# Optimization experiments

Measured on AMD Instinct MI355X. Metric: run time of the kernel, lower is better.

## Reference

```python
import jax, jax.numpy as jnp
import numpy as np

B, E, F, Q = 16, 2048, 8192, 20
D, WD = 256, 300
NUM_ENTITY, NUM_WORD, NUM_RELATION = 100000, 50000, 600
NUM_LAYER = 3
PAGERANK_LAMBDA = 0.8
FACT_SCALE = 3.0
VERY_NEG = -100000000000.0
VERY_SMALL = 1e-10


def setup_inputs() -> dict:
    key = jax.random.key(0)
    ks = jax.random.split(key, 40)
    s = 0.05
    L = NUM_LAYER
    inp = {
        'local_entity': jax.random.randint(ks[0], (B, E), 0, NUM_ENTITY),
        'q2e_adj_mat': jax.random.uniform(ks[1], (B, E, 1), jnp.float32),
        'kb_fact_rel': jax.random.randint(ks[2], (B, F), 0, NUM_RELATION),
        'query_text': jax.random.randint(ks[3], (B, Q), 0, NUM_WORD),
        'answer_dist': jax.random.uniform(ks[4], (B, E), jnp.float32),
        'e2f_ent': jax.random.randint(ks[5], (B, F), 0, E),
        'f2e_ent': jax.random.randint(ks[6], (B, F), 0, E),
        'word_emb': jax.random.normal(ks[7], (NUM_WORD + 1, WD)) * s,
        'entity_emb': jax.random.normal(ks[8], (NUM_ENTITY + 1, WD)) * s,
        'relation_emb': jax.random.normal(ks[9], (NUM_RELATION + 1, 2 * WD)) * s,
        'entity_lin_w': jax.random.normal(ks[10], (D, WD)) * s,
        'entity_lin_b': jnp.zeros((D,)),
        'relation_lin_w': jax.random.normal(ks[11], (D, 2 * WD)) * s,
        'relation_lin_b': jnp.zeros((D,)),
        'lstm_w_ih': jax.random.normal(ks[12], (4 * D, WD)) * s,
        'lstm_w_hh': jax.random.normal(ks[13], (4 * D, D)) * s,
        'lstm_b_ih': jnp.zeros((4 * D,)),
        'lstm_b_hh': jnp.zeros((4 * D,)),
        'q2e_w': jax.random.normal(ks[14], (L, D, D)) * s,
        'q2e_b': jnp.zeros((L, D)),
        'e2q_w': jax.random.normal(ks[15], (L, D, 3 * D)) * s,
        'e2q_b': jnp.zeros((L, D)),
        'e2e_w': jax.random.normal(ks[16], (L, D, 3 * D)) * s,
        'e2e_b': jnp.zeros((L, D)),
        'kb_head_w': jax.random.normal(ks[17], (L, D, D)) * s,
        'kb_head_b': jnp.zeros((L, D)),
        'kb_tail_w': jax.random.normal(ks[18], (L, D, D)) * s,
        'kb_tail_b': jnp.zeros((L, D)),
        'kb_self_w': jax.random.normal(ks[19], (L, D, D)) * s,
        'kb_self_b': jnp.zeros((L, D)),
        'score_w': jax.random.normal(ks[20], (1, D)) * s,
        'score_b': jnp.zeros((1,)),
    }
    return inp


def _lstm(x, w_ih, w_hh, b_ih, b_hh):
    # torch LSTM, single layer, unidirectional, zero init state; gates (i,f,g,o)
    gx = jnp.einsum('btd,gd->btg', x, w_ih) + b_ih + b_hh  # [B,T,4H]
    H = w_hh.shape[1]
    init = (jnp.zeros((x.shape[0], H), x.dtype), jnp.zeros((x.shape[0], H), x.dtype))
    def step(carry, g):
        h, c = carry
        z = g + h @ w_hh.T
        i, f, gg, o = jnp.split(z, 4, axis=-1)
        c = jax.nn.sigmoid(f) * c + jax.nn.sigmoid(i) * jnp.tanh(gg)
        h = jax.nn.sigmoid(o) * jnp.tanh(c)
        return (h, c), h
    (h, _), hs = jax.lax.scan(step, init, jnp.swapaxes(gx, 0, 1))
    return jnp.swapaxes(hs, 0, 1), h  # [B,T,H], [B,H]


def _forward(local_entity, q2e_adj_mat, kb_fact_rel, query_text, e2f_ent, f2e_ent,
             word_emb, entity_emb, relation_emb,
             entity_lin_w, entity_lin_b, relation_lin_w, relation_lin_b,
             lstm_w_ih, lstm_w_hh, lstm_b_ih, lstm_b_hh,
             q2e_w, q2e_b, e2q_w, e2q_b, e2e_w, e2e_b,
             kb_head_w, kb_head_b, kb_tail_w, kb_tail_b, kb_self_w, kb_self_b,
             score_w, score_b):
    bidx = jnp.arange(B)[:, None]
    ent_mask = (local_entity != NUM_ENTITY).astype(jnp.float32)  # [B,E]
    q_mask = (query_text != NUM_WORD).astype(jnp.float32)        # [B,Q]

    # query LSTM encoding (dropout = identity in eval)
    qh, qlast = _lstm(word_emb[query_text], lstm_w_ih, lstm_w_hh, lstm_b_ih, lstm_b_hh)
    query_node = qlast[:, None, :]                               # [B,1,D]

    # fact embeddings
    lf = relation_emb[kb_fact_rel] @ relation_lin_w.T + relation_lin_b  # [B,F,D]
    div = jnp.sqrt(jnp.float32(D))

    # fact <-> query attention
    sim = jnp.einsum('bqd,bfd->bqf', qh, lf) / div
    sim = jax.nn.softmax(sim + (1.0 - q_mask)[:, :, None] * VERY_NEG, axis=1)
    att = jnp.einsum('bqf,bqd->bfd', sim, qh)
    Wf = jnp.sum(att * lf, axis=2) / div                          # [B,F]
    W_tilde = jnp.exp(Wf - jnp.max(Wf, axis=1, keepdims=True))    # [B,F]

    # e2f softmax normalizer: scatter-add fact weights onto head entities
    e2f_softmax = jnp.zeros((B, E), W_tilde.dtype).at[bidx, e2f_ent].add(W_tilde)
    e2f_softmax = jnp.maximum(e2f_softmax, VERY_SMALL)

    # entity embeddings (word_dim != entity_dim -> linear projection)
    le = entity_emb[local_entity] @ entity_lin_w.T + entity_lin_b  # [B,E,D]
    pagerank = q2e_adj_mat[..., 0]                                 # [B,E]

    for i in range(NUM_LAYER):
        q2e = jnp.broadcast_to(query_node @ q2e_w[i].T + q2e_b[i], (B, E, D))
        # fact update: self + gathered head-entity messages
        fact_self = lf @ kb_self_w[i].T + kb_self_b[i]
        head = le @ kb_head_w[i].T + kb_head_b[i]
        e2f_emb = jax.nn.relu(fact_self + jnp.take_along_axis(head, e2f_ent[:, :, None], axis=1))
        norm = W_tilde * jnp.take_along_axis(pagerank / e2f_softmax, e2f_ent, axis=1)  # [B,F]
        e2f_emb = e2f_emb * norm[:, :, None]
        # entity update: self + scattered tail messages
        tail = e2f_emb @ kb_tail_w[i].T + kb_tail_b[i]
        ent_self = le @ kb_self_w[i].T + kb_self_b[i]
        f2e_emb = jax.nn.relu(ent_self + jnp.zeros((B, E, D), le.dtype).at[bidx, f2e_ent].add(tail))
        pagerank = (PAGERANK_LAMBDA * jnp.zeros((B, E), norm.dtype).at[bidx, f2e_ent].add(norm)
                    + (1.0 - PAGERANK_LAMBDA) * pagerank)
        nxt = jnp.concatenate([le, q2e, FACT_SCALE * f2e_emb], axis=2)  # [B,E,3D]
        query_node = jnp.einsum('be,bed->bd', pagerank, nxt @ e2q_w[i].T + e2q_b[i])[:, None, :]
        le = jax.nn.relu(nxt @ e2e_w[i].T + e2e_b[i])

    score = (le @ score_w.T + score_b)[..., 0]                     # [B,E]
    return score


def reference(local_entity, q2e_adj_mat, kb_fact_rel, query_text, answer_dist,
              e2f_ent, f2e_ent, word_emb, entity_emb, relation_emb,
              entity_lin_w, entity_lin_b, relation_lin_w, relation_lin_b,
              lstm_w_ih, lstm_w_hh, lstm_b_ih, lstm_b_hh,
              q2e_w, q2e_b, e2q_w, e2q_b, e2e_w, e2e_b,
              kb_head_w, kb_head_b, kb_tail_w, kb_tail_b, kb_self_w, kb_self_b,
              score_w, score_b):
    return _forward(local_entity, q2e_adj_mat, kb_fact_rel, query_text, e2f_ent, f2e_ent,
                    word_emb, entity_emb, relation_emb,
                    entity_lin_w, entity_lin_b, relation_lin_w, relation_lin_b,
                    lstm_w_ih, lstm_w_hh, lstm_b_ih, lstm_b_hh,
                    q2e_w, q2e_b, e2q_w, e2q_b, e2e_w, e2e_b,
                    kb_head_w, kb_head_b, kb_tail_w, kb_tail_b, kb_self_w, kb_self_b,
                    score_w, score_b)
```

## Files before the change

### kernel.cpp

```cpp
#include <hip/hip_runtime.h>
#include <hip/hip_bf16.h>

typedef __hip_bfloat16 bf16;
typedef __attribute__((ext_vector_type(8))) short bf16x8;
typedef __attribute__((ext_vector_type(4))) float f32x4;

#define BB 16
#define EE 2048
#define FF 8192
#define QQ 20
#define DD 256
#define WDIM 300
#define NWORD 50000
#define VERY_NEG_F (-1.0e11f)

static __device__ __forceinline__ float b2f(bf16 x){ return __bfloat162float(x); }
static __device__ __forceinline__ bf16 f2b(float x){ return __float2bfloat16(x); }
static __device__ __forceinline__ float sigm(float x){ return 1.f/(1.f+expf(-x)); }
static __device__ __forceinline__ void ld4bf(const bf16* p, float v[4]){
  short4 s = *(const short4*)p;
  v[0]=b2f(*(const bf16*)&s.x); v[1]=b2f(*(const bf16*)&s.y);
  v[2]=b2f(*(const bf16*)&s.z); v[3]=b2f(*(const bf16*)&s.w);
}
static __device__ __forceinline__ void st4bf(bf16* p, float a,float b,float c,float d){
  unsigned short u[4]; bf16 t;
  t=f2b(a);u[0]=*(unsigned short*)&t; t=f2b(b);u[1]=*(unsigned short*)&t;
  t=f2b(c);u[2]=*(unsigned short*)&t; t=f2b(d);u[3]=*(unsigned short*)&t;
  *(short4*)p=*(short4*)u;
}

#define O_GX       0UL
#define O_QH       1310720UL
#define O_QNODE    1638400UL
#define O_RELLIN   1654784UL
#define O_WR       2270208UL
#define O_WMAX     2308864UL
#define O_WT       2309120UL
#define O_E2FS     2833408UL
#define O_PR       2964480UL
#define O_PRAGG    3095552UL
#define O_Q2EV     3226624UL
#define O_Q2EVB    3243008UL
#define O_RELSELF  3251200UL
#define O_NORM     3866624UL
#define O_WNXT     4390912UL
#define O_PRSUM    4440064UL
#define O_CNT      4440320UL
#define O_CUR      4571392UL
#define O_BSTART   4702464UL
#define O_BIDX     4834048UL
#define O_ELWPAD   5358336UL
#define O_FLAG     5522176UL
#define O_CVT      5522432UL
#define O_AGG      10915584UL
#define O_ENTSELF  27692800UL
#define O_LEA      44470016UL
#define O_LEB      61247232UL
#define O_HEAD     78024448UL
#define O_F2EEMB   94801664UL

#define C_ELB   0
#define C_RLW   256
#define C_RLB   153856
#define C_WIH   154112
#define C_WHH   461312
#define C_BIH   723456
#define C_BHH   724480
#define C_Q2EW  725504
#define C_Q2EB  922112
#define C_E2QW  922880
#define C_E2QB  1512704
#define C_E2EW  1513472
#define C_E2EB  2103296
#define C_KHW   2104064
#define C_KHB   2300672
#define C_KTW   2301440
#define C_KTB   2498048
#define C_KSW   2498816
#define C_KSB   2695424
#define C_SCW   2696192
#define C_SCB   2696448

__global__ __launch_bounds__(256) void k_sniff(const unsigned short* ee, int* flag){
  __shared__ int red[256];
  int c=0;
  for(int i=threadIdx.x;i<4096;i+=256){
    int ex=(ee[2*i]>>7)&0xFF;
    c += (ex>=192);
  }
  red[threadIdx.x]=c; __syncthreads();
  for(int o=128;o;o>>=1){ if(threadIdx.x<o) red[threadIdx.x]+=red[threadIdx.x+o]; __syncthreads(); }
  if(!threadIdx.x) flag[0] = (red[0]>64) ? 1 : 0;
}

struct CvtJobs{ const void* src[20]; bf16* dst[20]; int n[20]; int sc[20]; };
__global__ __launch_bounds__(256) void k_cvt(CvtJobs J, const int* dfl){
  const int isf=*dfl;
  int j=blockIdx.y;
  int n=J.n[j];
  int i4=(blockIdx.x*256+threadIdx.x)*4;
  if(i4>=n) return;
  float m = (J.sc[j] && ((i4%768)>=512)) ? 3.f : 1.f;
  bf16* d=J.dst[j]+i4;
  if(isf){
    const float* s=(const float*)J.src[j]+i4;
    if(i4+4<=n){ float4 t=*(const float4*)s; st4bf(d,t.x*m,t.y*m,t.z*m,t.w*m); }
    else for(int r=0;i4+r<n;r++) d[r]=f2b(s[r]*m);
  } else {
    const bf16* s=(const bf16*)J.src[j]+i4;
    if(i4+4<=n){ float v[4]; ld4bf(s,v); st4bf(d,v[0]*m,v[1]*m,v[2]*m,v[3]*m); }
    else for(int r=0;i4+r<n;r++) d[r]=f2b(b2f(s[r])*m);
  }
}

__global__ __launch_bounds__(256) void k_cvtwhh(const void* src, bf16* wf, const int* dfl){
  const int isf=*dfl;
  int fid=blockIdx.x*256+threadIdx.x;
  int lane=fid&63, kt=(fid>>6)&7, gt=fid>>9;
  int l16=lane&15, q=lane>>4;
  long so=(long)(gt*16+l16)*256 + kt*32 + q*8;
  float v[8];
  if(isf){ const float* s=(const float*)src+so;
    #pragma unroll
    for(int j=0;j<8;j++) v[j]=s[j];
  } else { const bf16* s=(const bf16*)src+so; ld4bf(s,v); ld4bf(s+4,v+4); }
  bf16* d=wf+(long)fid*8;
  st4bf(d,v[0],v[1],v[2],v[3]); st4bf(d+4,v[4],v[5],v[6],v[7]);
}

__global__ __launch_bounds__(256) void k_cvtelw(const void* src, bf16* dst, const int* dfl){
  const int isf=*dfl;
  int r=blockIdx.x;
  for(int c=threadIdx.x;c<320;c+=256){
    float v=0.f;
    if(c<300) v = isf ? ((const float*)src)[r*300+c] : b2f(((const bf16*)src)[r*300+c]);
    dst[(long)r*320+c]=f2b(v);
  }
}

__global__ __launch_bounds__(128) void k_ga0(const int* idx, const void* emb, bf16* A0, const int* dfl){
  const int isf=*dfl;
  int row=blockIdx.x; int ent=idx[row]; int t=threadIdx.x;
  bf16* dst=A0+(long)row*320;
  if(t<75){
    float v[4];
    if(isf){ float4 x=*(const float4*)((const float*)emb+(long)ent*WDIM+t*4);
             v[0]=x.x;v[1]=x.y;v[2]=x.z;v[3]=x.w; }
    else ld4bf((const bf16*)emb+(long)ent*WDIM+t*4, v);
    st4bf(dst+t*4, v[0],v[1],v[2],v[3]);
  } else if(t<80){
    st4bf(dst+t*4, 0.f,0.f,0.f,0.f);
  }
}

__global__ __launch_bounds__(256) void k_cnt(const int* f2e, int* cnt){
  int i=blockIdx.x*256+threadIdx.x;
  atomicAdd(&cnt[((i>>13)<<11)+f2e[i]], 1);
}
__global__ __launch_bounds__(1024) void k_scan(const int* cnt, int* bstart){
  __shared__ int ps[1024];
  int t=threadIdx.x;
  int loc[32]; int s=0;
  #pragma unroll
  for(int j=0;j<32;j++){ loc[j]=s; s+=cnt[t*32+j]; }
  ps[t]=s; __syncthreads();
  for(int off=1;off<1024;off<<=1){
    int v=(t>=off)?ps[t-off]:0;
    __syncthreads(); ps[t]+=v; __syncthreads();
  }
  int base=(t? ps[t-1]:0);
  #pragma unroll
  for(int j=0;j<32;j++) bstart[t*32+j]=base+loc[j];
  if(t==1023) bstart[32768]=ps[1023];
}
__global__ __launch_bounds__(256) void k_fill(const int* f2e, const int* bstart, int* cur, int* bidx){
  int i=blockIdx.x*256+threadIdx.x;
  int key=((i>>13)<<11)+f2e[i];
  int pos=bstart[key]+atomicAdd(&cur[key],1);
  bidx[pos]=i;
}

__global__ __launch_bounds__(256) void k_gx(const int* qtext, const void* wemb,
    const bf16* wih, const bf16* bih, const bf16* bhh, float* gx, const int* dfl){
  const int isf=*dfl;
  int bt=blockIdx.x;
  __shared__ float xr[WDIM];
  int w=qtext[bt];
  for(int k4=threadIdx.x*4;k4<WDIM;k4+=1024){
    if(isf){ float4 t=*(const float4*)((const float*)wemb+(long)w*WDIM+k4);
             xr[k4]=t.x;xr[k4+1]=t.y;xr[k4+2]=t.z;xr[k4+3]=t.w; }
    else   { float v[4]; ld4bf((const bf16*)wemb+(long)w*WDIM+k4,v);
             xr[k4]=v[0];xr[k4+1]=v[1];xr[k4+2]=v[2];xr[k4+3]=v[3]; }
  }
  __syncthreads();
  #pragma unroll
  for(int s=0;s<4;s++){
    int g=threadIdx.x+256*s;
    float acc=b2f(bih[g])+b2f(bhh[g]);
    const bf16* wr=wih+(long)g*WDIM;
    for(int k4=0;k4<WDIM;k4+=4){
      float v[4]; ld4bf(wr+k4,v);
      acc+=v[0]*xr[k4]+v[1]*xr[k4+1]+v[2]*xr[k4+2]+v[3]*xr[k4+3];
    }
    gx[bt*1024+g]=acc;
  }
}

#define NLB 16
__global__ __launch_bounds__(256) void k_lstm3(const float* gx, const bf16* wf,
    float* qh, float* qnode, bf16* hbuf, int* lcnt){
  __shared__ bf16  hlds[16*264];
  __shared__ float zs[4*16*16];
  __shared__ bf16  hsl[256];
  const int k=blockIdx.x;
  const int tid=threadIdx.x;
  const int wv=tid>>6, lane=tid&63, q=lane>>4, l16=lane&15;
  const int b=tid>>4, u=tid&15, gu=k*16+u;
  bf16x8 wreg[8];
  #pragma unroll
  for(int kt=0;kt<8;kt++)
    wreg[kt]=*(const bf16x8*)(wf + (((long)((wv*16+k)*8+kt))*64 + lane)*8);
  float c=0.f;
  float gxr[4];
  #pragma unroll
  for(int g=0;g<4;g++) gxr[g]=gx[(b*QQ+0)*1024 + g*256 + gu];
  for(int t=0;t<QQ;t++){
    f32x4 acc=(f32x4){0.f,0.f,0.f,0.f};
    if(t){
      if(tid==0){
        while(__hip_atomic_load(lcnt+(t-1), __ATOMIC_ACQUIRE, __HIP_MEMORY_SCOPE_AGENT) < NLB)
          __builtin_amdgcn_s_sleep(1);
      }
      __syncthreads();
      const bf16* hb = hbuf + (t&1)*4096;
      #pragma unroll
      for(int ii=0;ii<4;ii++){
        int i=tid+ii*256;
        int r=i>>6, cc=i&63;
        unsigned long long v=__hip_atomic_load((const unsigned long long*)(hb + r*256 + cc*4),
                       __ATOMIC_RELAXED, __HIP_MEMORY_SCOPE_AGENT);
        *(unsigned long long*)&hlds[r*264 + cc*4] = v;
      }
      __syncthreads();
      #pragma unroll
      for(int kt=0;kt<8;kt++){
        bf16x8 af=*(const bf16x8*)&hlds[l16*264 + kt*32 + q*8];
        acc=__builtin_amdgcn_mfma_f32_16x16x32_bf16(af,wreg[kt],acc,0,0,0);
      }
    }
    #pragma unroll
    for(int r=0;r<4;r++) zs[wv*256 + (q*4+r)*16 + l16]=acc[r];
    __syncthreads();
    float zi=zs[0*256+tid]+gxr[0];
    float zf=zs[1*256+tid]+gxr[1];
    float zg=zs[2*256+tid]+gxr[2];
    float zo=zs[3*256+tid]+gxr[3];
    {
      int tn=(t<QQ-1)?t+1:t;
      #pragma unroll
      for(int g=0;g<4;g++) gxr[g]=gx[(b*QQ+tn)*1024 + g*256 + gu];
    }
    c=sigm(zf)*c+sigm(zi)*tanhf(zg);
    float hv=sigm(zo)*tanhf(c);
    hsl[tid]=f2b(hv);
    qh[(long)(b*QQ+t)*256+gu]=hv;
    if(t==QQ-1) qnode[(b<<8)+gu]=hv;
    __syncthreads();
    if(t<QQ-1){
      if(tid<64){
        bf16* hw=hbuf + ((t+1)&1)*4096;
        int bb=tid>>2, p=tid&3;
        unsigned long long v=*(unsigned long long*)&hsl[bb*16+p*4];
        __hip_atomic_store((unsigned long long*)(hw + bb*256 + k*16 + p*4), v,
                           __ATOMIC_RELAXED, __HIP_MEMORY_SCOPE_AGENT);
      }
      __syncthreads();
      if(tid==0){
        __threadfence();
        __hip_atomic_fetch_add(lcnt+t, 1, __ATOMIC_RELEASE, __HIP_MEMORY_SCOPE_AGENT);
      }
    }
  }
}

__global__ __launch_bounds__(256) void k_rel_lin(const void* remb, const bf16* rlw,
    const bf16* rlb, float* rel_lin, const int* dfl){
  const int isf=*dfl;
  int r=blockIdx.x;
  __shared__ float rr[2*WDIM];
  for(int k4=threadIdx.x*4;k4<2*WDIM;k4+=1024){
    if(isf){ float4 t=*(const float4*)((const float*)remb+(long)r*2*WDIM+k4);
             rr[k4]=t.x;rr[k4+1]=t.y;rr[k4+2]=t.z;rr[k4+3]=t.w; }
    else   { float v[4]; ld4bf((const bf16*)remb+(long)r*2*WDIM+k4,v);
             rr[k4]=v[0];rr[k4+1]=v[1];rr[k4+2]=v[2];rr[k4+3]=v[3]; }
  }
  __syncthreads();
  int d=threadIdx.x;
  float acc=b2f(rlb[d]);
  const bf16* wr=rlw+(long)d*2*WDIM;
  for(int k4=0;k4<2*WDIM;k4+=4){
    float v[4]; ld4bf(wr+k4,v);
    acc+=v[0]*rr[k4]+v[1]*rr[k4+1]+v[2]*rr[k4+2]+v[3]*rr[k4+3];
  }
  rel_lin[r*DD+d]=acc;
}

__global__ __launch_bounds__(256) void k_simwr(const float* qh, const float* rel_lin,
    const int* qtext, float* Wr){
  int b = blockIdx.x, rc = blockIdx.y;
  __shared__ float qhb[QQ*DD];
  __shared__ float qm[QQ];
  for(int i=threadIdx.x;i<QQ*DD;i+=256) qhb[i]=qh[b*QQ*DD+i];
  if(threadIdx.x<QQ) qm[threadIdx.x] = (qtext[b*QQ+threadIdx.x]!=NWORD)?0.f:VERY_NEG_F;
  __syncthreads();
  int r = rc*256+threadIdx.x;
  if(r>=601) return;
  float s[QQ];
  #pragma unroll
  for(int q=0;q<QQ;q++) s[q]=0.f;
  for(int k=0;k<DD;k++){
    float rl = rel_lin[r*DD+k];
    #pragma unroll
    for(int q=0;q<QQ;q++) s[q] += qhb[q*DD+k]*rl;
  }
  float m=-1e30f;
  #pragma unroll
  for(int q=0;q<QQ;q++){ s[q]*=0.0625f; m=fmaxf(m, s[q]+qm[q]); }
  float sum=0.f, w=0.f;
  #pragma unroll
  for(int q=0;q<QQ;q++){ float p=expf(s[q]+qm[q]-m); sum+=p; w+=p*s[q]; }
  Wr[b*601+r] = w/sum;
}

__global__ __launch_bounds__(256) void k_wmax(const float* Wr, const int* rel, float* wmax){
  int b=blockIdx.x; __shared__ float red[256];
  float m=-1e30f;
  for(int f=threadIdx.x;f<FF;f+=256) m=fmaxf(m, Wr[b*601+rel[b*FF+f]]);
  red[threadIdx.x]=m; __syncthreads();
  for(int o=128;o;o>>=1){ if(threadIdx.x<o) red[threadIdx.x]=fmaxf(red[threadIdx.x],red[threadIdx.x+o]); __syncthreads(); }
  if(!threadIdx.x) wmax[b]=red[0];
}
__global__ __launch_bounds__(256) void k_wt(const float* Wr, const int* rel,
    const float* wmax, const int* e2f, float* wt, float* e2fs){
  int i = blockIdx.x*256+threadIdx.x;
  int b = i>>13;
  float v = expf(Wr[b*601+rel[i]] - wmax[b]);
  wt[i]=v;
  atomicAdd(e2fs + (b<<11) + e2f[i], v);
}
__global__ __launch_bounds__(256) void k_prinit(const void* adj, float* pr, const int* dfl){
  const int isf=*dfl;
  int i4=(blockIdx.x*256+threadIdx.x)*4;
  if(isf){ *(float4*)(pr+i4)=*(const float4*)((const float*)adj+i4); }
  else { float v[4]; ld4bf((const bf16*)adj+i4,v);
         float4 t; t.x=v[0];t.y=v[1];t.z=v[2];t.w=v[3]; *(float4*)(pr+i4)=t; }
}

struct MG {
  const bf16* A; const bf16* W; const bf16* bias;
  bf16* out; int K;
  const bf16* Aq2; const bf16* Af2;
  const int* cnt; const bf16* addb;
};
template<int CONCAT,int EPI>
__global__ __launch_bounds__(256) void k_mgemm(MG p){
  const int m0 = blockIdx.x*64;
  const int wave = threadIdx.x>>6, lane = threadIdx.x&63;
  const int q = lane>>4, l16 = lane&15;
  const int n0 = wave*64;
  const int bidx_ = m0>>11;
  f32x4 acc[4][4];
  #pragma unroll
  for(int i=0;i<4;i++)
    #pragma unroll
    for(int j=0;j<4;j++) acc[i][j]=(f32x4){0.f,0.f,0.f,0.f};
  const int K=p.K;
  for(int k0=0;k0<K;k0+=32){
    int kk=k0+q*8;
    bf16x8 af[4], bw[4];
    #pragma unroll
    for(int mi=0;mi<4;mi++){
      int row=m0+mi*16+l16;
      const bf16* ap;
      if(CONCAT){
        if(kk<256)      ap=p.A  +(long)row*256+kk;
        else if(kk<512) ap=p.Aq2+(bidx_<<8)+(kk-256);
        else            ap=p.Af2+(long)row*256+(kk-512);
      } else ap=p.A+(long)row*K+kk;
      af[mi]=*(const bf16x8*)ap;
    }
    #pragma unroll
    for(int ni=0;ni<4;ni++)
      bw[ni]=*(const bf16x8*)(p.W+(long)(n0+ni*16+l16)*K+kk);
    #pragma unroll
    for(int mi=0;mi<4;mi++)
      #pragma unroll
      for(int ni=0;ni<4;ni++)
        acc[mi][ni]=__builtin_amdgcn_mfma_f32_16x16x32_bf16(af[mi],bw[ni],acc[mi][ni],0,0,0);
  }
  #pragma unroll
  for(int ni=0;ni<4;ni++){
    int col=n0+ni*16+l16;
    float bv=b2f(p.bias[col]);
    #pragma unroll
    for(int mi=0;mi<4;mi++){
      #pragma unroll
      for(int r=0;r<4;r++){
        int row=m0+mi*16+q*4+r;
        float v=acc[mi][ni][r];
        if(EPI==0) v+=bv;
        else if(EPI==1) v=fmaxf(v+bv,0.f);
        else {
          v += (float)p.cnt[row]*bv + b2f(p.addb[(long)row*256+col]);
          v=fmaxf(v,0.f);
        }
        p.out[(long)row*256+col]=f2b(v);
      }
    }
  }
}

__global__ __launch_bounds__(256) void k_small(const float* rel_lin, const bf16* selfw,
    const bf16* selfb, const float* qnode, const bf16* q2ew, const bf16* q2eb,
    float* relself, float* q2ev, bf16* q2evb){
  __shared__ float xr[DD];
  int d=threadIdx.x;
  if(blockIdx.x<601){
    int r=blockIdx.x;
    xr[d]=rel_lin[r*DD+d]; __syncthreads();
    float acc=b2f(selfb[d]);
    const bf16* wr=selfw+(long)d*DD;
    for(int k4=0;k4<DD;k4+=4){
      float v[4]; ld4bf(wr+k4,v);
      acc+=v[0]*xr[k4]+v[1]*xr[k4+1]+v[2]*xr[k4+2]+v[3]*xr[k4+3];
    }
    relself[r*DD+d]=acc;
  } else {
    int b=blockIdx.x-601;
    xr[d]=qnode[(b<<8)+d]; __syncthreads();
    float acc=b2f(q2eb[d]);
    const bf16* wr=q2ew+(long)d*DD;
    for(int k4=0;k4<DD;k4+=4){
      float v[4]; ld4bf(wr+k4,v);
      acc+=v[0]*xr[k4]+v[1]*xr[k4+1]+v[2]*xr[k4+2]+v[3]*xr[k4+3];
    }
    q2ev[(b<<8)+d]=acc;
    q2evb[(b<<8)+d]=f2b(acc);
  }
}

__global__ __launch_bounds__(256) void k_norm(const float* wt, const float* pr,
    const float* e2fs, const int* e2f, const int* f2e, float* normv, float* pragg){
  int i=blockIdx.x*256+threadIdx.x;
  int b=i>>13;
  int e=e2f[i];
  float v=wt[i]*pr[(b<<11)+e]/fmaxf(e2fs[(b<<11)+e],1e-10f);
  normv[i]=v;
  atomicAdd(pragg+(b<<11)+f2e[i], v);
}

__global__ __launch_bounds__(256) void k_agg(const int* bstart, const int* bidx,
    const int* rel, const int* e2f, const float* normv, const float* relself,
    const bf16* head, bf16* agg){
  int eidx=blockIdx.x*4+(threadIdx.x>>6);
  int lane=threadIdx.x&63;
  int b=eidx>>11;
  float a0=0.f,a1=0.f,a2=0.f,a3=0.f;
  int s=bstart[eidx], e=bstart[eidx+1];
  for(int i=s;i<e;i++){
    int f=bidx[i];
    int r=rel[f]; int ent=e2f[f]; float nv=normv[f];
    float4 rs=*(const float4*)&relself[r*DD+lane*4];
    float hd[4]; ld4bf(head+(long)(((b<<11)+ent)*DD+lane*4),hd);
    a0+=fmaxf(rs.x+hd[0],0.f)*nv; a1+=fmaxf(rs.y+hd[1],0.f)*nv;
    a2+=fmaxf(rs.z+hd[2],0.f)*nv; a3+=fmaxf(rs.w+hd[3],0.f)*nv;
  }
  st4bf(agg+(long)eidx*DD+lane*4, a0,a1,a2,a3);
}

__global__ __launch_bounds__(256) void k_wnxt(const float* pragg, float* pr, const bf16* le,
    const bf16* f2e, float* wnxt, float* prsum){
  __shared__ float r1[4*256];
  __shared__ float r3[4*256];
  __shared__ float rp[4];
  const int b=blockIdx.x, ch=blockIdx.y;
  const int wv=threadIdx.x>>6, lane=threadIdx.x&63;
  const int pe0=(b<<11)+ch*64+wv*16;
  float pv=0.f;
  if(lane<16){
    pv=0.8f*pragg[pe0+lane]+0.2f*pr[pe0+lane];
    pr[pe0+lane]=pv;
  }
  float a1[4]={0.f,0.f,0.f,0.f}, a3[4]={0.f,0.f,0.f,0.f}, ap=0.f;
  #pragma unroll
  for(int r=0;r<16;r++){
    float p=__shfl(pv, r, 64);
    long base=((long)(pe0+r))<<8;
    float v1[4],v3[4];
    ld4bf(le +base+lane*4, v1);
    ld4bf(f2e+base+lane*4, v3);
    #pragma unroll
    for(int j=0;j<4;j++){ a1[j]+=p*v1[j]; a3[j]+=p*v3[j]; }
    ap+=p;
  }
  #pragma unroll
  for(int j=0;j<4;j++){ r1[wv*256+lane*4+j]=a1[j]; r3[wv*256+lane*4+j]=a3[j]; }
  if(!lane) rp[wv]=ap;
  __syncthreads();
  const int t=threadIdx.x;
  float s1=r1[t]+r1[256+t]+r1[512+t]+r1[768+t];
  float s3=r3[t]+r3[256+t]+r3[512+t]+r3[768+t];
  atomicAdd(&wnxt[b*768+t], s1);
  atomicAdd(&wnxt[b*768+512+t], s3);
  if(!t) atomicAdd(&prsum[b], rp[0]+rp[1]+rp[2]+rp[3]);
}

__global__ __launch_bounds__(256) void k_qnode(const float* wnxt, const float* prsum,
    const float* q2ev, const bf16* w, const bf16* bias, float* qnode){
  int b=blockIdx.x, d=threadIdx.x;
  __shared__ float xr[768];
  float ps=prsum[b];
  xr[d]=wnxt[b*768+d];
  xr[256+d]=ps*q2ev[(b<<8)+d];
  xr[512+d]=wnxt[b*768+512+d];
  __syncthreads();
  float acc=0.f;
  const bf16* wr=w+(long)d*768;
  for(int k4=0;k4<768;k4+=4){
    float v[4]; ld4bf(wr+k4,v);
    acc+=v[0]*xr[k4]+v[1]*xr[k4+1]+v[2]*xr[k4+2]+v[3]*xr[k4+3];
  }
  qnode[(b<<8)+d]=acc+ps*b2f(bias[d]);
}

__global__ __launch_bounds__(256) void k_score(const bf16* le, const bf16* sw,
    const bf16* sb, void* out, const int* dfl){
  const int isf=*dfl;
  int o=blockIdx.x*4 + (threadIdx.x>>6);
  int lane=threadIdx.x&63;
  float v[4],wv[4];
  ld4bf(le+(long)o*DD+lane*4,v); ld4bf(sw+lane*4,wv);
  float acc=v[0]*wv[0]+v[1]*wv[1]+v[2]*wv[2]+v[3]*wv[3];
  for(int off=32;off;off>>=1) acc+=__shfl_down(acc,off,64);
  if(!lane){
    float r=acc+b2f(sb[0]);
    if(isf) ((float*)out)[o]=r; else ((bf16*)out)[o]=f2b(r);
  }
}

extern "C" void kernel_launch(void* const* d_in, const int* in_sizes, int n_in,
                              void* d_out, int out_size, void* d_ws, size_t ws_size,
                              hipStream_t stream){
  const int*  local_entity=(const int*)d_in[0];
  const void* q2e_adj     =d_in[1];
  const int*  kb_fact_rel =(const int*)d_in[2];
  const int*  query_text  =(const int*)d_in[3];
  const int*  e2f_ent     =(const int*)d_in[5];
  const int*  f2e_ent     =(const int*)d_in[6];
  const void* word_emb    =d_in[7];
  const void* entity_emb  =d_in[8];
  const void* relation_emb=d_in[9];

  char* ws=(char*)d_ws;
  float* gx      =(float*)(ws+O_GX);
  float* qh      =(float*)(ws+O_QH);
  float* qnode   =(float*)(ws+O_QNODE);
  float* rel_lin =(float*)(ws+O_RELLIN);
  float* Wr      =(float*)(ws+O_WR);
  float* wmax    =(float*)(ws+O_WMAX);
  float* wt      =(float*)(ws+O_WT);
  float* e2fs    =(float*)(ws+O_E2FS);
  float* pr      =(float*)(ws+O_PR);
  float* pragg   =(float*)(ws+O_PRAGG);
  float* q2ev    =(float*)(ws+O_Q2EV);
  bf16*  q2evb   =(bf16*)(ws+O_Q2EVB);
  float* relself =(float*)(ws+O_RELSELF);
  float* normv   =(float*)(ws+O_NORM);
  float* wnxt    =(float*)(ws+O_WNXT);
  float* prsum   =(float*)(ws+O_PRSUM);
  int*   cnt     =(int*)(ws+O_CNT);
  int*   cur     =(int*)(ws+O_CUR);
  int*   bstart  =(int*)(ws+O_BSTART);
  int*   bidx    =(int*)(ws+O_BIDX);
  bf16*  elwpad  =(bf16*)(ws+O_ELWPAD);
  int*   dflag   =(int*)(ws+O_FLAG);
  bf16*  cw      =(bf16*)(ws+O_CVT);
  bf16*  agg     =(bf16*)(ws+O_AGG);
  bf16*  A0      =(bf16*)(ws+O_AGG);
  bf16*  entself =(bf16*)(ws+O_ENTSELF);
  bf16*  leA     =(bf16*)(ws+O_LEA);
  bf16*  leB     =(bf16*)(ws+O_LEB);
  bf16*  headb   =(bf16*)(ws+O_HEAD);
  bf16*  f2eemb  =(bf16*)(ws+O_F2EEMB);
  bf16*  hbuf    =(bf16*)(ws+O_LEA);
  int*   lcnt    =(int*)(ws+O_LEA+16384);

  k_sniff<<<1,256,0,stream>>>((const unsigned short*)entity_emb, dflag);

  CvtJobs J;
  int cntj=0;
  auto add=[&](int in_idx, long coff, int n, int sc){
    J.src[cntj]=d_in[in_idx]; J.dst[cntj]=cw+coff; J.n[cntj]=n; J.sc[cntj]=sc; cntj++;
  };
  add(11,C_ELB,256,0);
  add(12,C_RLW,153600,0);  add(13,C_RLB,256,0);
  add(14,C_WIH,307200,0);
  add(16,C_BIH,1024,0);    add(17,C_BHH,1024,0);
  add(18,C_Q2EW,196608,0); add(19,C_Q2EB,768,0);
  add(20,C_E2QW,589824,1); add(21,C_E2QB,768,0);
  add(22,C_E2EW,589824,1); add(23,C_E2EB,768,0);
  add(24,C_KHW,196608,0);  add(25,C_KHB,768,0);
  add(26,C_KTW,196608,0);  add(27,C_KTB,768,0);
  add(28,C_KSW,196608,0);  add(29,C_KSB,768,0);
  add(30,C_SCW,256,0);     add(31,C_SCB,1,0);
  k_cvt<<<dim3(576,20),256,0,stream>>>(J, dflag);
  k_cvtwhh<<<128,256,0,stream>>>(d_in[15], cw+C_WHH, dflag);
  k_cvtelw<<<256,256,0,stream>>>(d_in[10], elwpad, dflag);

  hipMemsetAsync(cnt, 0, (size_t)2*BB*EE*4, stream);
  k_cnt <<<BB*FF/256,256,0,stream>>>(f2e_ent, cnt);
  k_scan<<<1,1024,0,stream>>>(cnt, bstart);
  k_fill<<<BB*FF/256,256,0,stream>>>(f2e_ent, bstart, cur, bidx);

  k_gx   <<<BB*QQ,256,0,stream>>>(query_text, word_emb, cw+C_WIH, cw+C_BIH, cw+C_BHH, gx, dflag);
  hipMemsetAsync(lcnt, 0, 128, stream);
  k_lstm3<<<NLB,256,0,stream>>>(gx, cw+C_WHH, qh, qnode, hbuf, lcnt);
  k_rel_lin<<<601,256,0,stream>>>(relation_emb, cw+C_RLW, cw+C_RLB, rel_lin, dflag);
  k_simwr<<<dim3(BB,3),256,0,stream>>>(qh, rel_lin, query_text, Wr);
  k_wmax <<<BB,256,0,stream>>>(Wr, kb_fact_rel, wmax);
  hipMemsetAsync(e2fs, 0, (size_t)BB*EE*4, stream);
  k_wt   <<<BB*FF/256,256,0,stream>>>(Wr, kb_fact_rel, wmax, e2f_ent, wt, e2fs);
  k_prinit<<<BB*EE/1024,256,0,stream>>>(q2e_adj, pr, dflag);

  k_ga0<<<BB*EE,128,0,stream>>>(local_entity, entity_emb, A0, dflag);
  {
    MG p{}; p.A=A0; p.W=elwpad; p.bias=cw+C_ELB; p.out=leA; p.K=320;
    k_mgemm<0,0><<<BB*EE/64,256,0,stream>>>(p);
  }

  bf16* le_cur=leA; bf16* le_nxt=leB;
  for(int i=0;i<3;i++){
    k_small<<<617,256,0,stream>>>(rel_lin, cw+C_KSW+(long)i*65536, cw+C_KSB+(long)i*256,
        qnode, cw+C_Q2EW+(long)i*65536, cw+C_Q2EB+(long)i*256, relself, q2ev, q2evb);
    {
      MG p{}; p.A=le_cur; p.W=cw+C_KHW+(long)i*65536; p.bias=cw+C_KHB+(long)i*256;
      p.out=headb; p.K=256;
      k_mgemm<0,0><<<BB*EE/64,256,0,stream>>>(p);
    }
    {
      MG p{}; p.A=le_cur; p.W=cw+C_KSW+(long)i*65536; p.bias=cw+C_KSB+(long)i*256;
      p.out=entself; p.K=256;
      k_mgemm<0,0><<<BB*EE/64,256,0,stream>>>(p);
    }
    hipMemsetAsync(pragg, 0, (size_t)BB*EE*4, stream);
    k_norm<<<BB*FF/256,256,0,stream>>>(wt, pr, e2fs, e2f_ent, f2e_ent, normv, pragg);
    k_agg <<<BB*EE/4,256,0,stream>>>(bstart, bidx, kb_fact_rel, e2f_ent, normv, relself, headb, agg);
    {
      MG p{}; p.A=agg; p.W=cw+C_KTW+(long)i*65536; p.bias=cw+C_KTB+(long)i*256;
      p.out=f2eemb; p.K=256; p.cnt=cnt; p.addb=entself;
      k_mgemm<0,2><<<BB*EE/64,256,0,stream>>>(p);
    }
    hipMemsetAsync(wnxt, 0, (size_t)(BB*768*4+256), stream);
    k_wnxt <<<dim3(BB,32),256,0,stream>>>(pragg, pr, le_cur, f2eemb, wnxt, prsum);
    k_qnode<<<BB,256,0,stream>>>(wnxt, prsum, q2ev, cw+C_E2QW+(long)i*196608, cw+C_E2QB+(long)i*256, qnode);
    {
      MG p{}; p.A=le_cur; p.W=cw+C_E2EW+(long)i*196608; p.bias=cw+C_E2EB+(long)i*256;
      p.out=le_nxt; p.K=768; p.Aq2=q2evb; p.Af2=f2eemb;
      k_mgemm<1,1><<<BB*EE/64,256,0,stream>>>(p);
    }
    bf16* t=le_cur; le_cur=le_nxt; le_nxt=t;
  }

  k_score<<<BB*EE/4,256,0,stream>>>(le_cur, cw+C_SCW, cw+C_SCB, d_out, dflag);
}
```

Before: 1.127 ms.

## Halve LSTM blocks, merge head/self GEMMs, and template GEMM K

The recurrent LSTM kernel now runs on 8 blocks of 512 threads instead of 16 blocks of 256. Every thread spin-waits with a relaxed load and then an acquire fence, and the per-step qh store moves after the cross-block signal as a nontemporal store. This is meant to cut the cost of the inter-block barrier on the serial critical path. The kb_head and kb_self GEMMs that share the same A operand are merged into one launch using a second grid dimension. The GEMM K dimension becomes a template parameter so the K loop can be fully unrolled, at the cost of more code and register pressure.

```diff
diff --git a/kernel.cpp b/kernel.cpp
--- a/kernel.cpp
+++ b/kernel.cpp
@@ -206,20 +206,20 @@
   }
 }
 
-#define NLB 16
-__global__ __launch_bounds__(256) void k_lstm3(const float* gx, const bf16* wf,
+#define NLB 8
+__global__ __launch_bounds__(512) void k_lstm4(const float* gx, const bf16* wf,
     float* qh, float* qnode, bf16* hbuf, int* lcnt){
   __shared__ bf16  hlds[16*264];
-  __shared__ float zs[4*16*16];
-  __shared__ bf16  hsl[256];
-  const int k=blockIdx.x;
-  const int tid=threadIdx.x;
+  __shared__ float zs[4*16*32];
+  __shared__ bf16  hsl[512];
+  const int k=blockIdx.x, tid=threadIdx.x;
   const int wv=tid>>6, lane=tid&63, q=lane>>4, l16=lane&15;
-  const int b=tid>>4, u=tid&15, gu=k*16+u;
+  const int gt=(wv>>1)*16 + k*2 + (wv&1);
+  const int b=tid>>5, u=tid&31, gu=k*32+u;
   bf16x8 wreg[8];
   #pragma unroll
   for(int kt=0;kt<8;kt++)
-    wreg[kt]=*(const bf16x8*)(wf + (((long)((wv*16+k)*8+kt))*64 + lane)*8);
+    wreg[kt]=*(const bf16x8*)(wf + (((long)(gt*8+kt))*64 + lane)*8);
   float c=0.f;
   float gxr[4];
   #pragma unroll
@@ -227,19 +227,19 @@
   for(int t=0;t<QQ;t++){
     f32x4 acc=(f32x4){0.f,0.f,0.f,0.f};
     if(t){
-      if(tid==0){
-        while(__hip_atomic_load(lcnt+(t-1), __ATOMIC_ACQUIRE, __HIP_MEMORY_SCOPE_AGENT) < NLB)
-          __builtin_amdgcn_s_sleep(1);
-      }
-      __syncthreads();
+      while(__hip_atomic_load(lcnt+(t-1), __ATOMIC_RELAXED, __HIP_MEMORY_SCOPE_AGENT) < NLB)
+        __builtin_amdgcn_s_sleep(2);
+      __builtin_amdgcn_fence(__ATOMIC_ACQUIRE, "agent");
+      __builtin_amdgcn_sched_barrier(0);
       const bf16* hb = hbuf + (t&1)*4096;
-      #pragma unroll
-      for(int ii=0;ii<4;ii++){
-        int i=tid+ii*256;
-        int r=i>>6, cc=i&63;
-        unsigned long long v=__hip_atomic_load((const unsigned long long*)(hb + r*256 + cc*4),
+      {
+        int r=tid>>5, cc=(tid&31)*8;
+        unsigned long long v0=__hip_atomic_load((const unsigned long long*)(hb + r*256 + cc),
                        __ATOMIC_RELAXED, __HIP_MEMORY_SCOPE_AGENT);
-        *(unsigned long long*)&hlds[r*264 + cc*4] = v;
+        unsigned long long v1=__hip_atomic_load((const unsigned long long*)(hb + r*256 + cc + 4),
+                       __ATOMIC_RELAXED, __HIP_MEMORY_SCOPE_AGENT);
+        *(unsigned long long*)&hlds[r*264 + cc] = v0;
+        *(unsigned long long*)&hlds[r*264 + cc + 4] = v1;
       }
       __syncthreads();
       #pragma unroll
@@ -249,12 +249,12 @@
       }
     }
     #pragma unroll
-    for(int r=0;r<4;r++) zs[wv*256 + (q*4+r)*16 + l16]=acc[r];
+    for(int r=0;r<4;r++) zs[(wv>>1)*512 + (q*4+r)*32 + (wv&1)*16 + l16]=acc[r];
     __syncthreads();
-    float zi=zs[0*256+tid]+gxr[0];
-    float zf=zs[1*256+tid]+gxr[1];
-    float zg=zs[2*256+tid]+gxr[2];
-    float zo=zs[3*256+tid]+gxr[3];
+    float zi=zs[0*512+b*32+u]+gxr[0];
+    float zf=zs[1*512+b*32+u]+gxr[1];
+    float zg=zs[2*512+b*32+u]+gxr[2];
+    float zo=zs[3*512+b*32+u]+gxr[3];
     {
       int tn=(t<QQ-1)?t+1:t;
       #pragma unroll
@@ -263,23 +263,21 @@
     c=sigm(zf)*c+sigm(zi)*tanhf(zg);
     float hv=sigm(zo)*tanhf(c);
     hsl[tid]=f2b(hv);
-    qh[(long)(b*QQ+t)*256+gu]=hv;
-    if(t==QQ-1) qnode[(b<<8)+gu]=hv;
     __syncthreads();
     if(t<QQ-1){
-      if(tid<64){
+      if(tid<128){
         bf16* hw=hbuf + ((t+1)&1)*4096;
-        int bb=tid>>2, p=tid&3;
-        unsigned long long v=*(unsigned long long*)&hsl[bb*16+p*4];
-        __hip_atomic_store((unsigned long long*)(hw + bb*256 + k*16 + p*4), v,
+        int bb=tid>>3, p=tid&7;
+        unsigned long long v=*(unsigned long long*)&hsl[bb*32+p*4];
+        __hip_atomic_store((unsigned long long*)(hw + bb*256 + k*32 + p*4), v,
                            __ATOMIC_RELAXED, __HIP_MEMORY_SCOPE_AGENT);
       }
       __syncthreads();
-      if(tid==0){
-        __threadfence();
+      if(tid==0)
         __hip_atomic_fetch_add(lcnt+t, 1, __ATOMIC_RELEASE, __HIP_MEMORY_SCOPE_AGENT);
-      }
-    }
+    }
+    __builtin_nontemporal_store(hv, &qh[(long)(b*QQ+t)*256+gu]);
+    if(t==QQ-1) qnode[(b<<8)+gu]=hv;
   }
 }
 
@@ -361,21 +359,24 @@
   bf16* out; int K;
   const bf16* Aq2; const bf16* Af2;
   const int* cnt; const bf16* addb;
+  const bf16* W2; const bf16* bias2; bf16* out2;
 };
-template<int CONCAT,int EPI>
+template<int CONCAT,int EPI,int TK,int DUAL>
 __global__ __launch_bounds__(256) void k_mgemm(MG p){
   const int m0 = blockIdx.x*64;
   const int wave = threadIdx.x>>6, lane = threadIdx.x&63;
   const int q = lane>>4, l16 = lane&15;
   const int n0 = wave*64;
   const int bidx_ = m0>>11;
+  const bf16* Wp = p.W; const bf16* biasp = p.bias; bf16* outp = p.out;
+  if(DUAL && blockIdx.y){ Wp=p.W2; biasp=p.bias2; outp=p.out2; }
   f32x4 acc[4][4];
   #pragma unroll
   for(int i=0;i<4;i++)
     #pragma unroll
     for(int j=0;j<4;j++) acc[i][j]=(f32x4){0.f,0.f,0.f,0.f};
-  const int K=p.K;
-  for(int k0=0;k0<K;k0+=32){
+  #pragma unroll
+  for(int k0=0;k0<TK;k0+=32){
     int kk=k0+q*8;
     bf16x8 af[4], bw[4];
     #pragma unroll
@@ -386,12 +387,12 @@
         if(kk<256)      ap=p.A  +(long)row*256+kk;
         else if(kk<512) ap=p.Aq2+(bidx_<<8)+(kk-256);
         else            ap=p.Af2+(long)row*256+(kk-512);
-      } else ap=p.A+(long)row*K+kk;
+      } else ap=p.A+(long)row*TK+kk;
       af[mi]=*(const bf16x8*)ap;
     }
     #pragma unroll
     for(int ni=0;ni<4;ni++)
-      bw[ni]=*(const bf16x8*)(p.W+(long)(n0+ni*16+l16)*K+kk);
+      bw[ni]=*(const bf16x8*)(Wp+(long)(n0+ni*16+l16)*TK+kk);
     #pragma unroll
     for(int mi=0;mi<4;mi++)
       #pragma unroll
@@ -401,7 +402,7 @@
   #pragma unroll
   for(int ni=0;ni<4;ni++){
     int col=n0+ni*16+l16;
-    float bv=b2f(p.bias[col]);
+    float bv=b2f(biasp[col]);
     #pragma unroll
     for(int mi=0;mi<4;mi++){
       #pragma unroll
@@ -414,7 +415,7 @@
           v += (float)p.cnt[row]*bv + b2f(p.addb[(long)row*256+col]);
           v=fmaxf(v,0.f);
         }
-        p.out[(long)row*256+col]=f2b(v);
+        outp[(long)row*256+col]=f2b(v);
       }
     }
   }
@@ -624,7 +625,7 @@
 
   k_gx   <<<BB*QQ,256,0,stream>>>(query_text, word_emb, cw+C_WIH, cw+C_BIH, cw+C_BHH, gx, dflag);
   hipMemsetAsync(lcnt, 0, 128, stream);
-  k_lstm3<<<NLB,256,0,stream>>>(gx, cw+C_WHH, qh, qnode, hbuf, lcnt);
+  k_lstm4<<<NLB,512,0,stream>>>(gx, cw+C_WHH, qh, qnode, hbuf, lcnt);
   k_rel_lin<<<601,256,0,stream>>>(relation_emb, cw+C_RLW, cw+C_RLB, rel_lin, dflag);
   k_simwr<<<dim3(BB,3),256,0,stream>>>(qh, rel_lin, query_text, Wr);
   k_wmax <<<BB,256,0,stream>>>(Wr, kb_fact_rel, wmax);
@@ -635,7 +636,7 @@
   k_ga0<<<BB*EE,128,0,stream>>>(local_entity, entity_emb, A0, dflag);
   {
     MG p{}; p.A=A0; p.W=elwpad; p.bias=cw+C_ELB; p.out=leA; p.K=320;
-    k_mgemm<0,0><<<BB*EE/64,256,0,stream>>>(p);
+    k_mgemm<0,0,320,0><<<BB*EE/64,256,0,stream>>>(p);
   }
 
   bf16* le_cur=leA; bf16* le_nxt=leB;
@@ -643,14 +644,10 @@
     k_small<<<617,256,0,stream>>>(rel_lin, cw+C_KSW+(long)i*65536, cw+C_KSB+(long)i*256,
         qnode, cw+C_Q2EW+(long)i*65536, cw+C_Q2EB+(long)i*256, relself, q2ev, q2evb);
     {
-      MG p{}; p.A=le_cur; p.W=cw+C_KHW+(long)i*65536; p.bias=cw+C_KHB+(long)i*256;
-      p.out=headb; p.K=256;
-      k_mgemm<0,0><<<BB*EE/64,256,0,stream>>>(p);
-    }
-    {
-      MG p{}; p.A=le_cur; p.W=cw+C_KSW+(long)i*65536; p.bias=cw+C_KSB+(long)i*256;
-      p.out=entself; p.K=256;
-      k_mgemm<0,0><<<BB*EE/64,256,0,stream>>>(p);
+      MG p{}; p.A=le_cur; p.K=256;
+      p.W=cw+C_KHW+(long)i*65536;  p.bias=cw+C_KHB+(long)i*256;  p.out=headb;
+      p.W2=cw+C_KSW+(long)i*65536; p.bias2=cw+C_KSB+(long)i*256; p.out2=entself;
+      k_mgemm<0,0,256,1><<<dim3(BB*EE/64,2),256,0,stream>>>(p);
     }
     hipMemsetAsync(pragg, 0, (size_t)BB*EE*4, stream);
     k_norm<<<BB*FF/256,256,0,stream>>>(wt, pr, e2fs, e2f_ent, f2e_ent, normv, pragg);
@@ -658,7 +655,7 @@
     {
       MG p{}; p.A=agg; p.W=cw+C_KTW+(long)i*65536; p.bias=cw+C_KTB+(long)i*256;
       p.out=f2eemb; p.K=256; p.cnt=cnt; p.addb=entself;
-      k_mgemm<0,2><<<BB*EE/64,256,0,stream>>>(p);
+      k_mgemm<0,2,256,0><<<BB*EE/64,256,0,stream>>>(p);
     }
     hipMemsetAsync(wnxt, 0, (size_t)(BB*768*4+256), stream);
     k_wnxt <<<dim3(BB,32),256,0,stream>>>(pragg, pr, le_cur, f2eemb, wnxt, prsum);
@@ -666,7 +663,7 @@
     {
       MG p{}; p.A=le_cur; p.W=cw+C_E2EW+(long)i*196608; p.bias=cw+C_E2EB+(long)i*256;
       p.out=le_nxt; p.K=768; p.Aq2=q2evb; p.Af2=f2eemb;
-      k_mgemm<1,1><<<BB*EE/64,256,0,stream>>>(p);
+      k_mgemm<1,1,768,0><<<BB*EE/64,256,0,stream>>>(p);
     }
     bf16* t=le_cur; le_cur=le_nxt; le_nxt=t;
   }
```

After: 1.118 ms. Within noise of the previous version (-0.8%).
